# Kernel optimization log

Measured on AMD Instinct MI355X. Metric: run time of the kernel, lower is better.

The kernel has to match this reference:

```python
import jax, jax.numpy as jnp
import numpy as np

B, S, IN_DIM, EMBED, HEADS, WINDOW = 2, 2048, 1024, 1024, 16, 256
HEAD_DIM = EMBED // HEADS
NEG_FILL = -9.0e15


def setup_inputs() -> dict:
    key = jax.random.key(0)
    k1, k2, k3, k4 = jax.random.split(key, 4)
    x = jax.random.normal(k1, (B, S, IN_DIM), dtype=jnp.float32)
    # padding_mask: positions with value 1 get zeroed in q/k/v (matches masked_fill semantics)
    padding_mask = jax.random.randint(k2, (B, S), 0, 2, dtype=jnp.int32)
    # xavier-uniform-like init scale for the linear weights
    lim_qkv = np.sqrt(6.0 / (IN_DIM + 3 * EMBED)).astype(np.float32)
    lim_o = np.sqrt(6.0 / (EMBED + EMBED)).astype(np.float32)
    Wqkv = jax.random.uniform(k3, (3 * EMBED, IN_DIM), jnp.float32, -lim_qkv, lim_qkv)
    bqkv = jnp.zeros((3 * EMBED,), jnp.float32)
    Wo = jax.random.uniform(k4, (EMBED, EMBED), jnp.float32, -lim_o, lim_o)
    bo = jnp.zeros((EMBED,), jnp.float32)
    return {"x": x, "padding_mask": padding_mask, "Wqkv": Wqkv, "bqkv": bqkv, "Wo": Wo, "bo": bo}


def reference(x, padding_mask, Wqkv, bqkv, Wo, bo):
    b, s, _ = x.shape
    h, hd, pad = HEADS, HEAD_DIM, WINDOW // 2
    # qkv projection: torch Linear is x @ W.T + b
    qkv = x @ Wqkv.T + bqkv                      # [B, S, 3E]
    qkv = qkv.reshape(b, s, h, 3 * hd).transpose(0, 2, 1, 3)  # [B, H, S, 3*hd]
    q, k, v = jnp.split(qkv, 3, axis=-1)          # each [B, H, S, hd]
    # zero out padded positions in q, k, v where padding_mask == 1
    pm = (padding_mask != 0)[:, None, :, None]    # [B, 1, S, 1]
    q = jnp.where(pm, 0.0, q)
    k = jnp.where(pm, 0.0, k)
    v = jnp.where(pm, 0.0, v)
    # dense banded scores: identical math to the unfold-based band compute
    scores = jnp.einsum("bhsd,bhtd->bhst", q, k)  # [B, H, S, S]
    idx = jnp.arange(s)
    band = jnp.abs(idx[None, :] - idx[:, None]) <= pad  # |i-j| <= window/2
    scores = jnp.where(band, scores, jnp.float32(NEG_FILL))
    scores = scores / jnp.sqrt(jnp.float32(hd))   # original scales AFTER the fill
    attn = jax.nn.softmax(scores, axis=-1)        # [B, H, S, S]
    vals = jnp.einsum("bhst,bhtd->bhsd", attn, v)  # [B, H, S, hd]
    vals = vals.transpose(0, 2, 1, 3).reshape(b, s, h * hd)  # [B, S, E]
    return vals @ Wo.T + bo
```

## Files before the change

### kernel.cpp

```cpp
#include <hip/hip_runtime.h>
#include <stdint.h>

#define S_LEN 2048
#define EMBED 1024
#define HEADS 16
#define HD 64
#define M_ROWS 4096
#define N_QKV 3072
#define KDIM 1024
#define SP 2336
#define CLP 136

typedef __attribute__((ext_vector_type(8))) short short8;
typedef __attribute__((ext_vector_type(4))) float f32x4;

__device__ __forceinline__ unsigned short f2bf(float f) {
  union { float f; uint32_t u; } c; c.f = f;
  uint32_t u = c.u;
  u += 0x7fffu + ((u >> 16) & 1u);
  return (unsigned short)(u >> 16);
}

__device__ __forceinline__ void gload_lds16(const unsigned short* g, unsigned short* l) {
  __builtin_amdgcn_global_load_lds(
      (const __attribute__((address_space(1))) void*)g,
      (__attribute__((address_space(3))) void*)l, 16, 0, 0);
}

#define XQ 1048576
#define WQKVQ 786432
#define WOQ 262144
#define CVTQ (XQ + WQKVQ + WOQ)
#define HALOQ 147456
__global__ __launch_bounds__(256) void cvt3_kernel(
    const float* __restrict__ x, const float* __restrict__ wqkv, const float* __restrict__ wo,
    unsigned short* __restrict__ xb, unsigned short* __restrict__ wqkvb, unsigned short* __restrict__ wob,
    unsigned short* __restrict__ vTp) {
  int i = blockIdx.x * blockDim.x + threadIdx.x;
  if (i < CVTQ) {
    const float* s; unsigned short* d; int off;
    if (i < XQ)               { s = x;    d = xb;    off = i; }
    else if (i < XQ + WQKVQ)  { s = wqkv; d = wqkvb; off = i - XQ; }
    else                      { s = wo;   d = wob;   off = i - XQ - WQKVQ; }
    float4 f = reinterpret_cast<const float4*>(s)[off];
    ushort4 o;
    o.x = f2bf(f.x); o.y = f2bf(f.y); o.z = f2bf(f.z); o.w = f2bf(f.w);
    reinterpret_cast<ushort4*>(d)[off] = o;
  } else {
    int j = i - CVTQ;
    int row = j / 72, p = j % 72;
    int off = row * 584 + (p < 32 ? p : 544 + (p - 32));
    reinterpret_cast<ushort4*>(vTp)[off] = (ushort4){0, 0, 0, 0};
  }
}

__global__ __launch_bounds__(256) void gemm_qkv(
    const unsigned short* __restrict__ A, const unsigned short* __restrict__ Bm,
    const float* __restrict__ bias, const int* __restrict__ pm,
    unsigned short* __restrict__ qo, unsigned short* __restrict__ ko,
    unsigned short* __restrict__ vTp)
{
  __shared__ __align__(16) unsigned short smem[12288];
  unsigned short* As = smem;
  unsigned short* Bs = smem + 4096;
  const int t = threadIdx.x, wave = t >> 6, lane = t & 63;
  const int m16 = lane & 15, q4 = lane >> 4;
  const int wm = wave >> 1, wn = wave & 1;
  const int flat = blockIdx.y * 24 + blockIdx.x;
  const int xcd = flat & 7, bi = flat >> 3;
  const int mb = (xcd & 3) * 16 + (bi & 15);
  const int nb = (xcd >> 2) * 12 + (bi >> 4);
  const int srow = lane >> 2, scol = (lane & 3) << 3;
  const unsigned short* pA  = A + (size_t)(mb * 64 + wave * 16 + srow) * KDIM + scol;
  const unsigned short* pB0 = Bm + (size_t)(nb * 128 + wave * 32 + srow) * KDIM + scol;
  const unsigned short* pB1 = Bm + (size_t)(nb * 128 + wave * 32 + 16 + srow) * KDIM + scol;
  f32x4 acc[2][4];
#pragma unroll
  for (int i_ = 0; i_ < 2; i_++)
#pragma unroll
    for (int j_ = 0; j_ < 4; j_++) acc[i_][j_] = (f32x4){0.f, 0.f, 0.f, 0.f};

  for (int kt = 0; kt < KDIM; kt += 64) {
    __syncthreads();
#pragma unroll
    for (int h = 0; h < 2; h++) {
      gload_lds16(pA + kt + h * 32,  As + h * 2048 + (wave * 16) * 32);
      gload_lds16(pB0 + kt + h * 32, Bs + h * 4096 + (wave * 32) * 32);
      gload_lds16(pB1 + kt + h * 32, Bs + h * 4096 + (wave * 32 + 16) * 32);
    }
    __syncthreads();
#pragma unroll
    for (int h = 0; h < 2; h++) {
      short8 af[2], bf[4];
#pragma unroll
      for (int mt = 0; mt < 2; mt++)
        af[mt] = *reinterpret_cast<const short8*>(&As[h * 2048 + (wm * 32 + mt * 16 + m16) * 32 + q4 * 8]);
#pragma unroll
      for (int nt = 0; nt < 4; nt++)
        bf[nt] = *reinterpret_cast<const short8*>(&Bs[h * 4096 + (wn * 64 + nt * 16 + m16) * 32 + q4 * 8]);
#pragma unroll
      for (int mt = 0; mt < 2; mt++)
#pragma unroll
        for (int nt = 0; nt < 4; nt++)
          acc[mt][nt] = __builtin_amdgcn_mfma_f32_16x16x32_bf16(af[mt], bf[nt], acc[mt][nt], 0, 0, 0);
    }
  }

  __syncthreads();
  float pmv[2][4];
#pragma unroll
  for (int mt = 0; mt < 2; mt++)
#pragma unroll
    for (int reg = 0; reg < 4; reg++) {
      int row = mb * 64 + wm * 32 + mt * 16 + q4 * 4 + reg;
      pmv[mt][reg] = (pm[row] != 0) ? 0.0f : 1.0f;
    }
#pragma unroll
  for (int nt = 0; nt < 4; nt++) {
    int cloc = wn * 64 + nt * 16 + m16;
    float bv = bias[nb * 128 + cloc];
#pragma unroll
    for (int mt = 0; mt < 2; mt++) {
#pragma unroll
      for (int reg = 0; reg < 4; reg++) {
        int rloc = wm * 32 + mt * 16 + q4 * 4 + reg;
        smem[rloc * CLP + cloc] = f2bf((acc[mt][nt][reg] + bv) * pmv[mt][reg]);
      }
    }
  }
  __syncthreads();
  {
    int part = t >> 6, r = t & 63;
    if (part < 2) {
      int g0 = nb * 128 + part * 64;
      int rem = g0 % 192, h = g0 / 192;
      if (rem < 128) {
        int s = mb * 64 + r;
        unsigned short* base = (rem == 0) ? qo : ko;
        unsigned short* dst = base + ((size_t)(((s >> 11) * 16 + h) * 2048 + (s & 2047))) * 64;
        const unsigned short* srcl = &smem[r * CLP + part * 64];
#pragma unroll
        for (int j = 0; j < 8; j++)
          *reinterpret_cast<short8*>(dst + j * 8) = *reinterpret_cast<const short8*>(srcl + j * 8);
      }
    } else {
      int nm3 = nb % 3;
      int vstart = (nm3 == 1) ? 0 : (nm3 == 2) ? 64 : -1;
      if (vstart >= 0) {
        int half = part - 2, c = vstart + r;
        int colg = nb * 128 + c, h = colg / 192, d = r;
        int s0 = mb * 64;
        int bh = (s0 >> 11) * 16 + h;
        unsigned short* dst = vTp + (size_t)(bh * 64 + d) * SP + 128 + (s0 & 2047) + half * 32;
#pragma unroll
        for (int j8 = 0; j8 < 4; j8++) {
          short8 tmp;
#pragma unroll
          for (int jj = 0; jj < 8; jj++)
            tmp[jj] = (short)smem[(half * 32 + j8 * 8 + jj) * CLP + c];
          *reinterpret_cast<short8*>(dst + j8 * 8) = tmp;
        }
      }
    }
  }
}

__global__ __launch_bounds__(256) void gemm_out(
    const unsigned short* __restrict__ A, const unsigned short* __restrict__ Bm,
    const float* __restrict__ bias, float* __restrict__ out)
{
  __shared__ __align__(16) unsigned char smemraw[17408];
  unsigned short* As = (unsigned short*)smemraw;
  unsigned short* Bs = As + 4096;
  float* Cldf = (float*)smemraw;
  const int t = threadIdx.x, wave = t >> 6, lane = t & 63;
  const int m16 = lane & 15, q4 = lane >> 4;
  const int wm = wave >> 1, wn = wave & 1;
  const int flat = blockIdx.y * 16 + blockIdx.x;
  const int xcd = flat & 7, bi = flat >> 3;
  const int mb = xcd * 8 + (bi & 7);
  const int nb = bi >> 3;
  const int srow = lane >> 2, scol = (lane & 3) << 3;
  const unsigned short* pA = A + (size_t)(mb * 64 + wave * 16 + srow) * KDIM + scol;
  const unsigned short* pB = Bm + (size_t)(nb * 64 + wave * 16 + srow) * KDIM + scol;
  f32x4 acc[2][2];
#pragma unroll
  for (int i_ = 0; i_ < 2; i_++)
#pragma unroll
    for (int j_ = 0; j_ < 2; j_++) acc[i_][j_] = (f32x4){0.f, 0.f, 0.f, 0.f};
  for (int kt = 0; kt < KDIM; kt += 64) {
    __syncthreads();
#pragma unroll
    for (int h = 0; h < 2; h++) {
      gload_lds16(pA + kt + h * 32, As + h * 2048 + (wave * 16) * 32);
      gload_lds16(pB + kt + h * 32, Bs + h * 2048 + (wave * 16) * 32);
    }
    __syncthreads();
#pragma unroll
    for (int h = 0; h < 2; h++) {
      short8 af[2], bf[2];
#pragma unroll
      for (int mt = 0; mt < 2; mt++)
        af[mt] = *reinterpret_cast<const short8*>(&As[h * 2048 + (wm * 32 + mt * 16 + m16) * 32 + q4 * 8]);
#pragma unroll
      for (int nt = 0; nt < 2; nt++)
        bf[nt] = *reinterpret_cast<const short8*>(&Bs[h * 2048 + (wn * 32 + nt * 16 + m16) * 32 + q4 * 8]);
#pragma unroll
      for (int mt = 0; mt < 2; mt++)
#pragma unroll
        for (int nt = 0; nt < 2; nt++)
          acc[mt][nt] = __builtin_amdgcn_mfma_f32_16x16x32_bf16(af[mt], bf[nt], acc[mt][nt], 0, 0, 0);
    }
  }
  __syncthreads();
#pragma unroll
  for (int nt = 0; nt < 2; nt++) {
    int cloc = wn * 32 + nt * 16 + m16;
    float bv = bias[nb * 64 + cloc];
#pragma unroll
    for (int mt = 0; mt < 2; mt++) {
#pragma unroll
      for (int reg = 0; reg < 4; reg++) {
        int rloc = wm * 32 + mt * 16 + q4 * 4 + reg;
        Cldf[rloc * 68 + cloc] = acc[mt][nt][reg] + bv;
      }
    }
  }
  __syncthreads();
  {
    int r = t >> 2, seg = t & 3;
    float* dst = out + (size_t)(mb * 64 + r) * EMBED + nb * 64 + seg * 16;
    const float* srcl = &Cldf[r * 68 + seg * 16];
#pragma unroll
    for (int j = 0; j < 4; j++)
      *reinterpret_cast<float4*>(dst + j * 4) = *reinterpret_cast<const float4*>(srcl + j * 4);
  }
}

__global__ __launch_bounds__(256, 4) void attn_kernel(
    const unsigned short* __restrict__ q, const unsigned short* __restrict__ k,
    const unsigned short* __restrict__ vTp, unsigned short* __restrict__ vals)
{
  __shared__ __align__(16) unsigned short Pld[4][16][296];
  const int bid = blockIdx.x;
  const int bh = bid & 31, qtg = bid >> 5;
  const int lane = threadIdx.x & 63, wave = threadIdx.x >> 6;
  const int qt = qtg * 4 + wave;
  const int i0 = qt * 16, w0 = i0 - 128;
  const int m16 = lane & 15, q4 = lane >> 4;

  const unsigned short* qb = q + ((size_t)(bh * 2048 + i0 + m16)) * 64 + q4 * 8;
  short8 aq0 = *reinterpret_cast<const short8*>(qb);
  short8 aq1 = *reinterpret_cast<const short8*>(qb + 32);

  float sum[4] = {0.f, 0.f, 0.f, 0.f};
#pragma unroll
  for (int ct = 0; ct < 18; ct++) {
    bool live = (ct < 17) && (w0 + ct * 16 + 15 >= 0) && (w0 + ct * 16 < 2048);
    if (live) {
      int js = w0 + ct * 16 + m16;
      int jc = js < 0 ? 0 : (js > 2047 ? 2047 : js);
      const unsigned short* kb = k + ((size_t)(bh * 2048 + jc)) * 64 + q4 * 8;
      short8 b0 = *reinterpret_cast<const short8*>(kb);
      short8 b1 = *reinterpret_cast<const short8*>(kb + 32);
      f32x4 a = {0.f, 0.f, 0.f, 0.f};
      a = __builtin_amdgcn_mfma_f32_16x16x32_bf16(aq0, b0, a, 0, 0, 0);
      a = __builtin_amdgcn_mfma_f32_16x16x32_bf16(aq1, b1, a, 0, 0, 0);
#pragma unroll
      for (int reg = 0; reg < 4; reg++) {
        int i = i0 + q4 * 4 + reg;
        bool valid = (js >= 0) && (js < 2048) && (js >= i - 128) && (js <= i + 128);
        float e = valid ? __expf(a[reg] * 0.125f) : 0.0f;
        sum[reg] += e;
        Pld[wave][q4 * 4 + reg][ct * 16 + m16] = f2bf(e);
      }
    } else {
#pragma unroll
      for (int reg = 0; reg < 4; reg++)
        Pld[wave][q4 * 4 + reg][ct * 16 + m16] = 0;
    }
  }
  float rden[4];
#pragma unroll
  for (int reg = 0; reg < 4; reg++) {
    float s = sum[reg];
    s += __shfl_xor(s, 1);
    s += __shfl_xor(s, 2);
    s += __shfl_xor(s, 4);
    s += __shfl_xor(s, 8);
    rden[reg] = 1.0f / s;
  }
  __syncthreads();
  short8 ap[9];
#pragma unroll
  for (int kc = 0; kc < 9; kc++)
    ap[kc] = *reinterpret_cast<const short8*>(&Pld[wave][m16][kc * 32 + q4 * 8]);

  const int b = bh >> 4, h = bh & 15;
#pragma unroll
  for (int dt = 0; dt < 4; dt++) {
    f32x4 av = {0.f, 0.f, 0.f, 0.f};
    const unsigned short* vb = vTp + ((size_t)(bh * 64 + dt * 16 + m16)) * SP + i0 + q4 * 8;
#pragma unroll
    for (int kc = 0; kc < 9; kc++) {
      short8 bv = *reinterpret_cast<const short8*>(vb + kc * 32);
      av = __builtin_amdgcn_mfma_f32_16x16x32_bf16(ap[kc], bv, av, 0, 0, 0);
    }
#pragma unroll
    for (int reg = 0; reg < 4; reg++)
      Pld[wave][q4 * 4 + reg][dt * 16 + m16] = f2bf(av[reg] * rden[reg]);
  }
  {
    int srow = lane >> 2, seg = lane & 3;
    unsigned short* dst = vals + ((size_t)(b * 2048 + i0 + srow)) * 1024 + h * 64 + seg * 16;
    const unsigned short* srcl = &Pld[wave][srow][seg * 16];
    *reinterpret_cast<short8*>(dst)     = *reinterpret_cast<const short8*>(srcl);
    *reinterpret_cast<short8*>(dst + 8) = *reinterpret_cast<const short8*>(srcl + 8);
  }
}

extern "C" void kernel_launch(void* const* d_in, const int* in_sizes, int n_in,
                              void* d_out, int out_size, void* d_ws, size_t ws_size,
                              hipStream_t stream) {
  const float* x    = (const float*)d_in[0];
  const int*   pm   = (const int*)d_in[1];
  const float* Wqkv = (const float*)d_in[2];
  const float* bqkv = (const float*)d_in[3];
  const float* Wo   = (const float*)d_in[4];
  const float* bo   = (const float*)d_in[5];
  float* out = (float*)d_out;
  char* ws = (char*)d_ws;

  unsigned short* xb    = (unsigned short*)(ws);
  unsigned short* vals  = (unsigned short*)(ws);
  unsigned short* Wqkvb = (unsigned short*)(ws +  8388608);
  unsigned short* Wob   = (unsigned short*)(ws + 14680064);
  unsigned short* qbuf  = (unsigned short*)(ws + 16777216);
  unsigned short* kbuf  = (unsigned short*)(ws + 25165824);
  unsigned short* vTp   = (unsigned short*)(ws + 33554432);

  cvt3_kernel<<<8768, 256, 0, stream>>>(x, Wqkv, Wo, xb, Wqkvb, Wob, vTp);
  gemm_qkv<<<dim3(24, 64), 256, 0, stream>>>(xb, Wqkvb, bqkv, pm, qbuf, kbuf, vTp);
  attn_kernel<<<1024, 256, 0, stream>>>(qbuf, kbuf, vTp, vals);
  gemm_out<<<dim3(16, 64), 256, 0, stream>>>(vals, Wob, bo, out);
}
```

Baseline: 179.5 us.

## Widen QKV GEMM tile to one full head (64x192) and simplify epilogue scatter

The QKV GEMM tile grows from 64x128 to 64x192 so that each block covers exactly one head's q, k and v columns. The epilogue therefore loses its branching and every thread writes q, k and the transposed v. The grid becomes 1024 blocks, and the XCD-aware block swizzle is replaced by a plain linear mapping. Each block holds more accumulators and uses more LDS, which could lower occupancy, and dropping the swizzle may hurt L2 locality.

```diff
diff --git a/kernel.cpp b/kernel.cpp
--- a/kernel.cpp
+++ b/kernel.cpp
@@ -9,7 +9,7 @@
 #define N_QKV 3072
 #define KDIM 1024
 #define SP 2336
-#define CLP 136
+#define CLP2 200
 
 typedef __attribute__((ext_vector_type(8))) short short8;
 typedef __attribute__((ext_vector_type(4))) float f32x4;
@@ -31,7 +31,6 @@
 #define WQKVQ 786432
 #define WOQ 262144
 #define CVTQ (XQ + WQKVQ + WOQ)
-#define HALOQ 147456
 __global__ __launch_bounds__(256) void cvt3_kernel(
     const float* __restrict__ x, const float* __restrict__ wqkv, const float* __restrict__ wo,
     unsigned short* __restrict__ xb, unsigned short* __restrict__ wqkvb, unsigned short* __restrict__ wob,
@@ -60,48 +59,48 @@
     unsigned short* __restrict__ qo, unsigned short* __restrict__ ko,
     unsigned short* __restrict__ vTp)
 {
-  __shared__ __align__(16) unsigned short smem[12288];
+  __shared__ __align__(16) unsigned short smem[16384];
   unsigned short* As = smem;
   unsigned short* Bs = smem + 4096;
   const int t = threadIdx.x, wave = t >> 6, lane = t & 63;
   const int m16 = lane & 15, q4 = lane >> 4;
   const int wm = wave >> 1, wn = wave & 1;
-  const int flat = blockIdx.y * 24 + blockIdx.x;
-  const int xcd = flat & 7, bi = flat >> 3;
-  const int mb = (xcd & 3) * 16 + (bi & 15);
-  const int nb = (xcd >> 2) * 12 + (bi >> 4);
+  const int bid = blockIdx.x;
+  const int mb = bid >> 4, nb = bid & 15;
   const int srow = lane >> 2, scol = (lane & 3) << 3;
-  const unsigned short* pA  = A + (size_t)(mb * 64 + wave * 16 + srow) * KDIM + scol;
-  const unsigned short* pB0 = Bm + (size_t)(nb * 128 + wave * 32 + srow) * KDIM + scol;
-  const unsigned short* pB1 = Bm + (size_t)(nb * 128 + wave * 32 + 16 + srow) * KDIM + scol;
-  f32x4 acc[2][4];
+  const unsigned short* pA = A + (size_t)(mb * 64 + wave * 16 + srow) * KDIM + scol;
+  const unsigned short* pB0 = Bm + (size_t)(nb * 192 + wave * 48 + srow) * KDIM + scol;
+  const unsigned short* pB1 = Bm + (size_t)(nb * 192 + wave * 48 + 16 + srow) * KDIM + scol;
+  const unsigned short* pB2 = Bm + (size_t)(nb * 192 + wave * 48 + 32 + srow) * KDIM + scol;
+  f32x4 acc[2][6];
 #pragma unroll
   for (int i_ = 0; i_ < 2; i_++)
 #pragma unroll
-    for (int j_ = 0; j_ < 4; j_++) acc[i_][j_] = (f32x4){0.f, 0.f, 0.f, 0.f};
+    for (int j_ = 0; j_ < 6; j_++) acc[i_][j_] = (f32x4){0.f, 0.f, 0.f, 0.f};
 
   for (int kt = 0; kt < KDIM; kt += 64) {
     __syncthreads();
 #pragma unroll
     for (int h = 0; h < 2; h++) {
       gload_lds16(pA + kt + h * 32,  As + h * 2048 + (wave * 16) * 32);
-      gload_lds16(pB0 + kt + h * 32, Bs + h * 4096 + (wave * 32) * 32);
-      gload_lds16(pB1 + kt + h * 32, Bs + h * 4096 + (wave * 32 + 16) * 32);
+      gload_lds16(pB0 + kt + h * 32, Bs + h * 6144 + (wave * 48) * 32);
+      gload_lds16(pB1 + kt + h * 32, Bs + h * 6144 + (wave * 48 + 16) * 32);
+      gload_lds16(pB2 + kt + h * 32, Bs + h * 6144 + (wave * 48 + 32) * 32);
     }
     __syncthreads();
 #pragma unroll
     for (int h = 0; h < 2; h++) {
-      short8 af[2], bf[4];
+      short8 af[2], bf[6];
 #pragma unroll
       for (int mt = 0; mt < 2; mt++)
         af[mt] = *reinterpret_cast<const short8*>(&As[h * 2048 + (wm * 32 + mt * 16 + m16) * 32 + q4 * 8]);
 #pragma unroll
-      for (int nt = 0; nt < 4; nt++)
-        bf[nt] = *reinterpret_cast<const short8*>(&Bs[h * 4096 + (wn * 64 + nt * 16 + m16) * 32 + q4 * 8]);
+      for (int nt = 0; nt < 6; nt++)
+        bf[nt] = *reinterpret_cast<const short8*>(&Bs[h * 6144 + (wn * 96 + nt * 16 + m16) * 32 + q4 * 8]);
 #pragma unroll
       for (int mt = 0; mt < 2; mt++)
 #pragma unroll
-        for (int nt = 0; nt < 4; nt++)
+        for (int nt = 0; nt < 6; nt++)
           acc[mt][nt] = __builtin_amdgcn_mfma_f32_16x16x32_bf16(af[mt], bf[nt], acc[mt][nt], 0, 0, 0);
     }
   }
@@ -116,52 +115,43 @@
       pmv[mt][reg] = (pm[row] != 0) ? 0.0f : 1.0f;
     }
 #pragma unroll
-  for (int nt = 0; nt < 4; nt++) {
-    int cloc = wn * 64 + nt * 16 + m16;
-    float bv = bias[nb * 128 + cloc];
+  for (int nt = 0; nt < 6; nt++) {
+    int cloc = wn * 96 + nt * 16 + m16;
+    float bv = bias[nb * 192 + cloc];
 #pragma unroll
     for (int mt = 0; mt < 2; mt++) {
 #pragma unroll
       for (int reg = 0; reg < 4; reg++) {
         int rloc = wm * 32 + mt * 16 + q4 * 4 + reg;
-        smem[rloc * CLP + cloc] = f2bf((acc[mt][nt][reg] + bv) * pmv[mt][reg]);
+        smem[rloc * CLP2 + cloc] = f2bf((acc[mt][nt][reg] + bv) * pmv[mt][reg]);
       }
     }
   }
   __syncthreads();
+  const int s0 = mb * 64;
+  const int bh = (s0 >> 11) * 16 + nb, s0l = s0 & 2047;
   {
-    int part = t >> 6, r = t & 63;
-    if (part < 2) {
-      int g0 = nb * 128 + part * 64;
-      int rem = g0 % 192, h = g0 / 192;
-      if (rem < 128) {
-        int s = mb * 64 + r;
-        unsigned short* base = (rem == 0) ? qo : ko;
-        unsigned short* dst = base + ((size_t)(((s >> 11) * 16 + h) * 2048 + (s & 2047))) * 64;
-        const unsigned short* srcl = &smem[r * CLP + part * 64];
-#pragma unroll
-        for (int j = 0; j < 8; j++)
-          *reinterpret_cast<short8*>(dst + j * 8) = *reinterpret_cast<const short8*>(srcl + j * 8);
-      }
-    } else {
-      int nm3 = nb % 3;
-      int vstart = (nm3 == 1) ? 0 : (nm3 == 2) ? 64 : -1;
-      if (vstart >= 0) {
-        int half = part - 2, c = vstart + r;
-        int colg = nb * 128 + c, h = colg / 192, d = r;
-        int s0 = mb * 64;
-        int bh = (s0 >> 11) * 16 + h;
-        unsigned short* dst = vTp + (size_t)(bh * 64 + d) * SP + 128 + (s0 & 2047) + half * 32;
-#pragma unroll
-        for (int j8 = 0; j8 < 4; j8++) {
-          short8 tmp;
-#pragma unroll
-          for (int jj = 0; jj < 8; jj++)
-            tmp[jj] = (short)smem[(half * 32 + j8 * 8 + jj) * CLP + c];
-          *reinterpret_cast<short8*>(dst + j8 * 8) = tmp;
-        }
-      }
-    }
+    int r = t >> 2, seg = t & 3;
+    const unsigned short* sq = &smem[r * CLP2 + seg * 16];
+    unsigned short* dq = qo + ((size_t)(bh * 2048 + s0l + r)) * 64 + seg * 16;
+    *reinterpret_cast<short8*>(dq)     = *reinterpret_cast<const short8*>(sq);
+    *reinterpret_cast<short8*>(dq + 8) = *reinterpret_cast<const short8*>(sq + 8);
+    const unsigned short* sk = &smem[r * CLP2 + 64 + seg * 16];
+    unsigned short* dk = ko + ((size_t)(bh * 2048 + s0l + r)) * 64 + seg * 16;
+    *reinterpret_cast<short8*>(dk)     = *reinterpret_cast<const short8*>(sk);
+    *reinterpret_cast<short8*>(dk + 8) = *reinterpret_cast<const short8*>(sk + 8);
+  }
+  {
+    int d = t & 63, qtr = t >> 6;
+    short8 tmp0, tmp1;
+#pragma unroll
+    for (int jj = 0; jj < 8; jj++) {
+      tmp0[jj] = (short)smem[(qtr * 16 + jj) * CLP2 + 128 + d];
+      tmp1[jj] = (short)smem[(qtr * 16 + 8 + jj) * CLP2 + 128 + d];
+    }
+    unsigned short* dst = vTp + (size_t)(bh * 64 + d) * SP + 128 + s0l + qtr * 16;
+    *reinterpret_cast<short8*>(dst)     = tmp0;
+    *reinterpret_cast<short8*>(dst + 8) = tmp1;
   }
 }
 
@@ -340,7 +330,7 @@
   unsigned short* vTp   = (unsigned short*)(ws + 33554432);
 
   cvt3_kernel<<<8768, 256, 0, stream>>>(x, Wqkv, Wo, xb, Wqkvb, Wob, vTp);
-  gemm_qkv<<<dim3(24, 64), 256, 0, stream>>>(xb, Wqkvb, bqkv, pm, qbuf, kbuf, vTp);
+  gemm_qkv<<<1024, 256, 0, stream>>>(xb, Wqkvb, bqkv, pm, qbuf, kbuf, vTp);
   attn_kernel<<<1024, 256, 0, stream>>>(qbuf, kbuf, vTp, vals);
   gemm_out<<<dim3(16, 64), 256, 0, stream>>>(vals, Wob, bo, out);
 }
```

Measured after the change: 183.0 us. About the same (+1.9%).
